# Optimization experiments

Measured on AMD Instinct MI355X. Metric: run time of the kernel, lower is better.

The kernel has to match this reference:

```python
import jax, jax.numpy as jnp
import numpy as np

TEMPERATURE = 0.1   # g.temperature
THRESHOLD = 0.05    # g.init_threshold
B, LEN_S, LEN_E = 8, 50, 10   # batch, sentence positions, max_word_length
N = B * LEN_S * LEN_E         # number of candidate spans
VOCAB = 30000


def setup_inputs() -> dict:
    key = jax.random.key(0)
    k0, k1 = jax.random.split(key)
    # positive edit-distance-like scores between every candidate span and every vocab word
    ed_dist = jax.random.uniform(k0, (N, VOCAB), dtype=jnp.float32) * 10.0
    flat = jnp.arange(N, dtype=jnp.int64)
    bi = flat // (LEN_S * LEN_E)          # batch index of each candidate
    lsi = (flat // LEN_E) % LEN_S         # start index
    lei = flat % LEN_E                    # (length-1) index
    viable = jax.random.uniform(k1, (N,)) < 0.5
    return {"ed_dist": ed_dist, "bi": bi, "lsi": lsi, "lei": lei, "viable": viable}


def _soft_min(x, axis):
    # w = (-x / T).log_softmax().exp(); value = (x * w).sum; index = argmin
    w = jax.nn.softmax(-x / TEMPERATURE, axis=axis)
    return (x * w).sum(axis), jnp.argmin(x, axis=axis)


def _soft_max(x, axis):
    w = jax.nn.softmax(x / TEMPERATURE, axis=axis)
    return (x * w).sum(axis), jnp.argmax(x, axis=axis)


def _celu(x):  # alpha = 1
    return jnp.where(x > 0, x, jnp.expm1(jnp.minimum(x, 0.0)))


def _soft_threshold(x, thresh):
    return (_celu(1.0 - 2.0 * x / thresh) + 1.0) / 2.0


def _restore_shape(tensor, bi, lsi, lei, viable, value):
    # scatter viable candidates into dense (B, LEN_S, LEN_E); non-viable go to a dump slot
    flat_idx = bi * (LEN_S * LEN_E) + lsi * LEN_E + lei
    dump = B * LEN_S * LEN_E
    idx = jnp.where(viable, flat_idx, dump)
    ret = jnp.full((dump + 1,), value, dtype=tensor.dtype)
    ret = ret.at[idx].set(tensor)
    return ret[:-1].reshape(B, LEN_S, LEN_E)


def reference(ed_dist, bi, lsi, lei, viable):
    # soft-min over vocab: best matched edit distance + hard vocab index
    matched_ed, matched_vocab = _soft_min(ed_dist, axis=-1)
    # soft thresholding to matching score
    matched_thresh = _soft_threshold(matched_ed, THRESHOLD)
    # restore dense (batch, len_s, len_e) shape
    score_dense = _restore_shape(matched_thresh, bi, lsi, lei, viable, 0.0)
    vocab_dense = _restore_shape(matched_vocab, bi, lsi, lei, viable, jnp.array(-1, matched_vocab.dtype))
    # soft-max over all spans per batch element
    flat_scores = score_dense.reshape(B, LEN_S * LEN_E)
    best_matched_score, best_idx = _soft_max(flat_scores, axis=-1)
    best_matched_vocab = jnp.take_along_axis(
        vocab_dense.reshape(B, LEN_S * LEN_E), best_idx[:, None], axis=1)[:, 0]
    start = best_idx // LEN_E
    end = start + best_idx % LEN_E
    return best_matched_score, start, end, best_matched_vocab, score_dense
```

## Files before the change

kernel.cpp:

```cpp
#include <hip/hip_runtime.h>
#include <stdint.h>

#define NROWS 4000
#define NCOLS 30000
#define NQ4   1875
#define BATCH 8
#define SPANS 500
#define LEN_E_ 10
#define KLOG2E 14.4269504088896340736f

__device__ __forceinline__ float fexp2(float x) {
    return __builtin_amdgcn_exp2f(x);
}

__global__ __launch_bounds__(256) void softmin_rows(
    const float* __restrict__ ed, float* __restrict__ out,
    int* __restrict__ amin) {
    const int row = blockIdx.x;
    const int tid = threadIdx.x;

    const float4* __restrict__ rp =
        (const float4*)(ed + (size_t)row * NCOLS);

    float Z = 0.f, S = 0.f, mv = INFINITY;
    int   vi = 0;

    for (int j = tid; j < NQ4; j += 256) {
        float4 vv[4];
        vv[0] = rp[4 * j + 0];
        vv[1] = rp[4 * j + 1];
        vv[2] = rp[4 * j + 2];
        vv[3] = rp[4 * j + 3];
        const int base = j << 4;
#pragma unroll
        for (int q = 0; q < 4; ++q) {
#pragma unroll
            for (int c = 0; c < 4; ++c) {
                float x = (&vv[q].x)[c];
                float e = fexp2(x * -KLOG2E);
                Z += e;
                S = fmaf(x, e, S);
                bool lt = x < mv;
                mv = lt ? x : mv;
                vi = lt ? (base + q * 4 + c) : vi;
            }
        }
    }

#pragma unroll
    for (int off = 32; off > 0; off >>= 1) {
        Z += __shfl_down(Z, off);
        S += __shfl_down(S, off);
        float ov = __shfl_down(mv, off);
        int   oi = __shfl_down(vi, off);
        if (ov < mv || (ov == mv && oi < vi)) { mv = ov; vi = oi; }
    }
    __shared__ float wZ[4], wS[4], wM[4];
    __shared__ int   wI[4];
    if ((tid & 63) == 0) {
        int w = tid >> 6;
        wZ[w] = Z; wS[w] = S; wM[w] = mv; wI[w] = vi;
    }
    __syncthreads();

    if (tid == 0) {
        float Zt = 0.f, St = 0.f, m = INFINITY;
        int ii = 0;
#pragma unroll
        for (int w = 0; w < 4; ++w) {
            Zt += wZ[w]; St += wS[w];
            if (wM[w] < m || (wM[w] == m && wI[w] < ii)) { m = wM[w]; ii = wI[w]; }
        }
        float ed_v  = St / Zt;
        float z     = 1.f - 40.f * ed_v;
        float celu  = z > 0.f ? z : expm1f(z);
        amin[row]     = ii;
        out[32 + row] = 0.5f * (celu + 1.f);
    }
}

__global__ __launch_bounds__(512) void finish(
    const void* __restrict__ viable, const int* __restrict__ amin,
    float* __restrict__ out) {
    const int tid  = threadIdx.x;
    const int wid  = tid >> 6;
    const int lane = tid & 63;

    __shared__ int s_esz;
    if (tid < 64) {
        const uint8_t* p = (const uint8_t*)viable;
        int c = 0;
#pragma unroll
        for (int k = 0; k < 32; ++k) c += (p[tid * 32 + k] != 0);
#pragma unroll
        for (int off = 32; off > 0; off >>= 1) c += __shfl_down(c, off);
        if (tid == 0) s_esz = (c >= 800) ? 1 : (c >= 192 ? 4 : 8);
    }
    __syncthreads();
    const int esz = s_esz;

    const int b = wid;
    float* __restrict__ sc = out + 32 + b * SPANS;

    float xs[8];
    float mx = -INFINITY; int ai = 0;
#pragma unroll
    for (int k = 0; k < 8; ++k) {
        int j = lane + k * 64;
        float xm = 0.f;
        if (j < SPANS) {
            float s = sc[j];
            int   gi = b * SPANS + j;
            bool viab;
            if (esz == 1)      viab = ((const uint8_t*)viable)[gi] != 0;
            else if (esz == 4) viab = ((const uint32_t*)viable)[gi] != 0u;
            else               viab = ((const unsigned long long*)viable)[gi] != 0ull;
            xm = viab ? s : 0.f;
            sc[j] = xm;
            if (xm > mx) { mx = xm; ai = j; }
        }
        xs[k] = xm;
    }

#pragma unroll
    for (int off = 32; off > 0; off >>= 1) {
        float ov = __shfl_xor(mx, off);
        int   oi = __shfl_xor(ai, off);
        if (ov > mx || (ov == mx && oi < ai)) { mx = ov; ai = oi; }
    }
    const float M    = mx;
    const int   best = ai;

    float Z = 0.f, S = 0.f;
#pragma unroll
    for (int k = 0; k < 8; ++k) {
        int j = lane + k * 64;
        if (j < SPANS) {
            float e = fexp2((xs[k] - M) * KLOG2E);
            Z += e;
            S = fmaf(xs[k], e, S);
        }
    }
#pragma unroll
    for (int off = 32; off > 0; off >>= 1) {
        Z += __shfl_xor(Z, off);
        S += __shfl_xor(S, off);
    }

    if (lane == 0) {
        int start = best / LEN_E_;
        int len   = best % LEN_E_;
        out[b]      = S / Z;
        out[8 + b]  = (float)start;
        out[16 + b] = (float)(start + len);
        out[24 + b] = (M > 0.f) ? (float)amin[b * SPANS + best] : -1.f;
    }
}

extern "C" void kernel_launch(void* const* d_in, const int* in_sizes, int n_in,
                              void* d_out, int out_size, void* d_ws,
                              size_t ws_size, hipStream_t stream) {
    const float* ed     = (const float*)d_in[0];
    const void*  viable = d_in[4];
    float* out  = (float*)d_out;
    int*   amin = (int*)d_ws;

    hipLaunchKernelGGL(softmin_rows, dim3(NROWS), dim3(256), 0, stream,
                       ed, out, amin);
    hipLaunchKernelGGL(finish, dim3(1), dim3(512), 0, stream,
                       viable, amin, out);
}
```

Measured before the change: 95.05 us.

## Use one wavefront per row for softmin and one block per batch in finish

The row softmin kernel now launches a single 64-lane wavefront per row instead of four wavefronts. The shared-memory cross-wave combine and the block barrier go away, but each lane handles four times as many float4 groups. The finishing kernel now uses 8 blocks of 256 threads, one per batch element, and reduces through shared memory with barriers instead of wave shuffles. The main risk is less memory-level parallelism per row in the bandwidth-bound pass, although 4000 rows still give many wavefronts.

```diff
diff --git a/kernel.cpp b/kernel.cpp
--- a/kernel.cpp
+++ b/kernel.cpp
@@ -13,11 +13,11 @@
     return __builtin_amdgcn_exp2f(x);
 }
 
-__global__ __launch_bounds__(256) void softmin_rows(
+__global__ __launch_bounds__(64) void softmin_rows(
     const float* __restrict__ ed, float* __restrict__ out,
     int* __restrict__ amin) {
-    const int row = blockIdx.x;
-    const int tid = threadIdx.x;
+    const int row  = blockIdx.x;
+    const int lane = threadIdx.x;
 
     const float4* __restrict__ rp =
         (const float4*)(ed + (size_t)row * NCOLS);
@@ -25,7 +25,7 @@
     float Z = 0.f, S = 0.f, mv = INFINITY;
     int   vi = 0;
 
-    for (int j = tid; j < NQ4; j += 256) {
+    for (int j = lane; j < NQ4; j += 64) {
         float4 vv[4];
         vv[0] = rp[4 * j + 0];
         vv[1] = rp[4 * j + 1];
@@ -55,36 +55,21 @@
         int   oi = __shfl_down(vi, off);
         if (ov < mv || (ov == mv && oi < vi)) { mv = ov; vi = oi; }
     }
-    __shared__ float wZ[4], wS[4], wM[4];
-    __shared__ int   wI[4];
-    if ((tid & 63) == 0) {
-        int w = tid >> 6;
-        wZ[w] = Z; wS[w] = S; wM[w] = mv; wI[w] = vi;
-    }
-    __syncthreads();
 
-    if (tid == 0) {
-        float Zt = 0.f, St = 0.f, m = INFINITY;
-        int ii = 0;
-#pragma unroll
-        for (int w = 0; w < 4; ++w) {
-            Zt += wZ[w]; St += wS[w];
-            if (wM[w] < m || (wM[w] == m && wI[w] < ii)) { m = wM[w]; ii = wI[w]; }
-        }
-        float ed_v  = St / Zt;
+    if (lane == 0) {
+        float ed_v  = S / Z;
         float z     = 1.f - 40.f * ed_v;
         float celu  = z > 0.f ? z : expm1f(z);
-        amin[row]     = ii;
+        amin[row]     = vi;
         out[32 + row] = 0.5f * (celu + 1.f);
     }
 }
 
-__global__ __launch_bounds__(512) void finish(
+__global__ __launch_bounds__(256) void span_softmax(
     const void* __restrict__ viable, const int* __restrict__ amin,
     float* __restrict__ out) {
-    const int tid  = threadIdx.x;
-    const int wid  = tid >> 6;
-    const int lane = tid & 63;
+    const int b   = blockIdx.x;
+    const int tid = threadIdx.x;
 
     __shared__ int s_esz;
     if (tid < 64) {
@@ -99,58 +84,68 @@
     __syncthreads();
     const int esz = s_esz;
 
-    const int b = wid;
     float* __restrict__ sc = out + 32 + b * SPANS;
 
-    float xs[8];
+    float x0 = 0.f, x1 = 0.f;
     float mx = -INFINITY; int ai = 0;
-#pragma unroll
-    for (int k = 0; k < 8; ++k) {
-        int j = lane + k * 64;
-        float xm = 0.f;
+    {
+        int j = tid;
         if (j < SPANS) {
             float s = sc[j];
-            int   gi = b * SPANS + j;
+            int gi = b * SPANS + j;
             bool viab;
             if (esz == 1)      viab = ((const uint8_t*)viable)[gi] != 0;
             else if (esz == 4) viab = ((const uint32_t*)viable)[gi] != 0u;
             else               viab = ((const unsigned long long*)viable)[gi] != 0ull;
-            xm = viab ? s : 0.f;
-            sc[j] = xm;
-            if (xm > mx) { mx = xm; ai = j; }
+            x0 = viab ? s : 0.f;
+            sc[j] = x0;
+            if (x0 > mx) { mx = x0; ai = j; }
         }
-        xs[k] = xm;
+        j = tid + 256;
+        if (j < SPANS) {
+            float s = sc[j];
+            int gi = b * SPANS + j;
+            bool viab;
+            if (esz == 1)      viab = ((const uint8_t*)viable)[gi] != 0;
+            else if (esz == 4) viab = ((const uint32_t*)viable)[gi] != 0u;
+            else               viab = ((const unsigned long long*)viable)[gi] != 0ull;
+            x1 = viab ? s : 0.f;
+            sc[j] = x1;
+            if (x1 > mx) { mx = x1; ai = j; }
+        }
     }
 
-#pragma unroll
-    for (int off = 32; off > 0; off >>= 1) {
-        float ov = __shfl_xor(mx, off);
-        int   oi = __shfl_xor(ai, off);
-        if (ov > mx || (ov == mx && oi < ai)) { mx = ov; ai = oi; }
+    __shared__ float sv[256], sZ[256], sS[256];
+    __shared__ int   si[256];
+    sv[tid] = mx; si[tid] = ai;
+    __syncthreads();
+    for (int off = 128; off > 0; off >>= 1) {
+        if (tid < off) {
+            float v2 = sv[tid+off]; int i2 = si[tid+off];
+            if (v2 > sv[tid] || (v2 == sv[tid] && i2 < si[tid])) {
+                sv[tid] = v2; si[tid] = i2;
+            }
+        }
+        __syncthreads();
     }
-    const float M    = mx;
-    const int   best = ai;
+    const float M    = sv[0];
+    const int   best = si[0];
+    __syncthreads();
 
     float Z = 0.f, S = 0.f;
-#pragma unroll
-    for (int k = 0; k < 8; ++k) {
-        int j = lane + k * 64;
-        if (j < SPANS) {
-            float e = fexp2((xs[k] - M) * KLOG2E);
-            Z += e;
-            S = fmaf(xs[k], e, S);
-        }
-    }
-#pragma unroll
-    for (int off = 32; off > 0; off >>= 1) {
-        Z += __shfl_xor(Z, off);
-        S += __shfl_xor(S, off);
+    if (tid < SPANS)       { float e = fexp2((x0 - M) * KLOG2E); Z += e; S = fmaf(x0, e, S); }
+    if (tid + 256 < SPANS) { float e = fexp2((x1 - M) * KLOG2E); Z += e; S = fmaf(x1, e, S); }
+    sZ[tid] = Z; sS[tid] = S;
+    __syncthreads();
+    for (int off = 128; off > 0; off >>= 1) {
+        if (tid < off) { sZ[tid] += sZ[tid+off]; sS[tid] += sS[tid+off]; }
+        __syncthreads();
     }
 
-    if (lane == 0) {
+    if (tid == 0) {
         int start = best / LEN_E_;
         int len   = best % LEN_E_;
-        out[b]      = S / Z;
+        out[b]      = sS[0] / sZ[0];
         out[8 + b]  = (float)start;
         out[16 + b] = (float)(start + len);
         out[24 + b] = (M > 0.f) ? (float)amin[b * SPANS + best] : -1.f;
@@ -165,8 +160,8 @@
     float* out  = (float*)d_out;
     int*   amin = (int*)d_ws;
 
-    hipLaunchKernelGGL(softmin_rows, dim3(NROWS), dim3(256), 0, stream,
+    hipLaunchKernelGGL(softmin_rows, dim3(NROWS), dim3(64), 0, stream,
                        ed, out, amin);
-    hipLaunchKernelGGL(finish, dim3(1), dim3(512), 0, stream,
+    hipLaunchKernelGGL(span_softmax, dim3(BATCH), dim3(256), 0, stream,
                        viable, amin, out);
 }
```

Measured after the change: 96.94 us. No clear change (+2.0%).
